# Kernel optimization log

Hardware: AMD Instinct MI355X
Metric: run time of the kernel (lower is better)

The kernel has to match this reference:

```python
import jax, jax.numpy as jnp
import numpy as np
import math

D_MODEL = 1024
N_HEADS = 16
FACTOR = 5
B, L, S = 8, 4096, 4096
U = FACTOR * int(math.log(L))  # 40 sampled queries


def setup_inputs() -> dict:
    key = jax.random.key(0)
    ks = jax.random.split(key, 12)
    scale_w = 1.0 / math.sqrt(D_MODEL)
    return {
        "queries": jax.random.normal(ks[0], (B, L, D_MODEL), dtype=jnp.float32),
        "keys": jax.random.normal(ks[1], (B, S, D_MODEL), dtype=jnp.float32),
        "values": jax.random.normal(ks[2], (B, S, D_MODEL), dtype=jnp.float32),
        "Wq": jax.random.normal(ks[3], (D_MODEL, D_MODEL), dtype=jnp.float32) * scale_w,
        "bq": jnp.zeros((D_MODEL,), dtype=jnp.float32),
        "Wk": jax.random.normal(ks[4], (D_MODEL, D_MODEL), dtype=jnp.float32) * scale_w,
        "bk": jnp.zeros((D_MODEL,), dtype=jnp.float32),
        "Wv": jax.random.normal(ks[5], (D_MODEL, D_MODEL), dtype=jnp.float32) * scale_w,
        "bv": jnp.zeros((D_MODEL,), dtype=jnp.float32),
        "Wo": jax.random.normal(ks[6], (D_MODEL, D_MODEL), dtype=jnp.float32) * scale_w,
        "bo": jnp.zeros((D_MODEL,), dtype=jnp.float32),
        "sample_index": jax.random.randint(ks[7], (U,), 0, L, dtype=jnp.int64 if jax.config.jax_enable_x64 else jnp.int32),
    }


def reference(queries, keys, values, Wq, bq, Wk, bk, Wv, bv, Wo, bo, sample_index):
    H, E = N_HEADS, D_MODEL // N_HEADS
    scale = D_MODEL ** (-0.5)  # module uses d_model**-0.5, not d_head**-0.5

    # Projections (torch Linear: y = x @ W.T + b)
    Q = (jnp.einsum('bld,od->blo', queries, Wq) + bq).reshape(B, L, H, E)
    K = (jnp.einsum('bsd,od->bso', keys, Wk) + bk).reshape(B, S, H, E)
    V = (jnp.einsum('bsd,od->bso', values, Wv) + bv).reshape(B, S, H, E)

    # ProbSparse query sampling: gather U = factor*log(L) queries
    Qs = Q[:, sample_index, :, :]  # [B, U, H, E]

    # SDPA on the reduced query set
    scores = jnp.einsum('buhe,bshe->bhus', Qs, K) * scale  # [B, H, U, S]
    attn = jax.nn.softmax(scores, axis=-1)
    out = jnp.einsum('bhus,bshe->buhe', attn, V).reshape(B, U, D_MODEL)

    out = jnp.einsum('bud,od->buo', out, Wo) + bo  # [B, U, D_MODEL]
    return out, attn
```

## Files before the change

### kernel.cpp

```cpp
#include <hip/hip_runtime.h>
#include <stdint.h>

#define DM  1024
#define NB  8
#define LQ  4096
#define SSQ 4096
#define NH  16
#define HE  64
#define UU  40
#define NS  8
#define SPL (SSQ/NS)

using u16 = unsigned short;
using u32 = unsigned int;

typedef __bf16 bf16x8 __attribute__((ext_vector_type(8)));
typedef float  f32x4  __attribute__((ext_vector_type(4)));

#define AS1 __attribute__((address_space(1)))
#define AS3 __attribute__((address_space(3)))

__device__ __forceinline__ void gld_lds16(const void* g, void* l) {
  __builtin_amdgcn_global_load_lds((const AS1 u32*)g, (AS3 u32*)l, 16, 0, 0);
}

__device__ __forceinline__ u16 f2bf(float x) {
  u32 u = __float_as_uint(x);
  u32 r = (u + 0x7fffu + ((u >> 16) & 1u)) >> 16;
  return (u16)r;
}

__global__ __launch_bounds__(256)
void conv_bf16(const float* __restrict__ src, u16* __restrict__ dst, long n) {
  long i = ((long)blockIdx.x * 256 + threadIdx.x) * 8;
  if (i >= n) return;
  float4 a = *(const float4*)(src + i);
  float4 b = *(const float4*)(src + i + 4);
  union { u16 h[8]; uint4 v; } pk;
  pk.h[0]=f2bf(a.x); pk.h[1]=f2bf(a.y); pk.h[2]=f2bf(a.z); pk.h[3]=f2bf(a.w);
  pk.h[4]=f2bf(b.x); pk.h[5]=f2bf(b.y); pk.h[6]=f2bf(b.z); pk.h[7]=f2bf(b.w);
  *(uint4*)(dst + i) = pk.v;
}

struct WPtrs {
  const float* s0; const float* s1; const float* s2; const float* s3;
  u16* d0; u16* d1; u16* d2; u16* d3;
};
__global__ __launch_bounds__(256)
void conv_w4(WPtrs p) {
  int wsel = blockIdx.y;
  const float* s = wsel==0 ? p.s0 : wsel==1 ? p.s1 : wsel==2 ? p.s2 : p.s3;
  u16*         d = wsel==0 ? p.d0 : wsel==1 ? p.d1 : wsel==2 ? p.d2 : p.d3;
  long i = ((long)blockIdx.x * 256 + threadIdx.x) * 8;
  float4 a = *(const float4*)(s + i);
  float4 b = *(const float4*)(s + i + 4);
  union { u16 h[8]; uint4 v; } pk;
  pk.h[0]=f2bf(a.x); pk.h[1]=f2bf(a.y); pk.h[2]=f2bf(a.z); pk.h[3]=f2bf(a.w);
  pk.h[4]=f2bf(b.x); pk.h[5]=f2bf(b.y); pk.h[6]=f2bf(b.z); pk.h[7]=f2bf(b.w);
  *(uint4*)(d + i) = pk.v;
}

__global__ __launch_bounds__(128)
void gather_q_bf16(const float* __restrict__ q, const int* __restrict__ sidx,
                   u16* __restrict__ dst) {
  int r = blockIdx.x;
  int b = r / UU, u = r - b*UU;
  long srow = ((long)b*LQ + sidx[u]) * DM;
  int c = threadIdx.x * 8;
  float4 a = *(const float4*)(q + srow + c);
  float4 bb = *(const float4*)(q + srow + c + 4);
  union { u16 h[8]; uint4 v; } pk;
  pk.h[0]=f2bf(a.x); pk.h[1]=f2bf(a.y); pk.h[2]=f2bf(a.z); pk.h[3]=f2bf(a.w);
  pk.h[4]=f2bf(bb.x); pk.h[5]=f2bf(bb.y); pk.h[6]=f2bf(bb.z); pk.h[7]=f2bf(bb.w);
  *(uint4*)(dst + (long)r*DM + c) = pk.v;
}

template<bool BIAS_ROW, bool MINOR_N>
__global__ __launch_bounds__(512, 2)
void gemm256(const u16* __restrict__ Ab, const u16* __restrict__ Bb,
             const float* __restrict__ bias, u16* __restrict__ Cb,
             int mTiles, int nTiles, long ldo)
{
  __shared__ u16 lds[2][2][256*64];
  const int t = threadIdx.x;
  const int l = t & 63;
  const int w = t >> 6;
  const int wr = w >> 2, wc = w & 3;

  const int nwg = mTiles * nTiles;
  const int bid = blockIdx.x;
  const int wg = (bid & 7) * (nwg >> 3) + (bid >> 3);
  int xm, yn;
  if (MINOR_N) { xm = wg / nTiles; yn = wg - xm*nTiles; }
  else         { yn = wg / mTiles; xm = wg - yn*mTiles; }
  const int r0 = xm * 256, o0 = yn * 256;

  const int srow = t >> 3, sslot = t & 7;
  const int scol = (sslot ^ (srow & 7)) * 8;
  const long aoff = (long)(r0 + srow) * DM + scol;
  const long boff = (long)(o0 + srow) * DM + scol;

  f32x4 acc[8][4];
  const f32x4 z4 = {0.f,0.f,0.f,0.f};
#pragma unroll
  for (int m = 0; m < 8; m++)
#pragma unroll
    for (int n = 0; n < 4; n++) acc[m][n] = z4;

  const int swz   = (l & 7) << 4;
  const int klane = (l >> 4) << 4;
  const int arow0 = wr*128 + (l & 15);
  const int brow0 = wc*64  + (l & 15);

  auto stage = [&](int tile, int buf) {
#pragma unroll
    for (int j = 0; j < 4; j++)
      gld_lds16(Ab + aoff + (long)j*(64*DM) + tile*64,
                (char*)&lds[buf][0][0] + (512*j + 64*w)*16);
#pragma unroll
    for (int j = 0; j < 4; j++)
      gld_lds16(Bb + boff + (long)j*(64*DM) + tile*64,
                (char*)&lds[buf][1][0] + (512*j + 64*w)*16);
  };

  stage(0, 0);
  __syncthreads();

  for (int tt = 0; tt < 16; tt++) {
    const int cur = tt & 1;
    if (tt < 15) stage(tt+1, cur^1);
    const char* Abase = (const char*)&lds[cur][0][0];
    const char* Bbase = (const char*)&lds[cur][1][0];
#pragma unroll
    for (int kk = 0; kk < 2; kk++) {
      const int cb = (kk*64 + klane) ^ swz;
      bf16x8 af[8], bf[4];
#pragma unroll
      for (int m = 0; m < 8; m++)
        af[m] = *(const bf16x8*)(Abase + (arow0 + m*16)*128 + cb);
#pragma unroll
      for (int n = 0; n < 4; n++)
        bf[n] = *(const bf16x8*)(Bbase + (brow0 + n*16)*128 + cb);
      __builtin_amdgcn_s_setprio(1);
#pragma unroll
      for (int m = 0; m < 8; m++)
#pragma unroll
        for (int n = 0; n < 4; n++)
          acc[m][n] = __builtin_amdgcn_mfma_f32_16x16x32_bf16(af[m], bf[n], acc[m][n], 0, 0, 0);
      __builtin_amdgcn_s_setprio(0);
    }
    __syncthreads();
  }

  float* eps = (float*)((char*)&lds[0][0][0] + w*8704);
  const int colg = o0 + wc*64 + (l & 7)*8;
  float bc[8];
  if (!BIAS_ROW) {
    float4 b0 = *(const float4*)&bias[colg];
    float4 b1 = *(const float4*)&bias[colg + 4];
    bc[0]=b0.x; bc[1]=b0.y; bc[2]=b0.z; bc[3]=b0.w;
    bc[4]=b1.x; bc[5]=b1.y; bc[6]=b1.z; bc[7]=b1.w;
  }
  const int fq = l >> 4;
  const int fr16 = l & 15;
#pragma unroll
  for (int mc = 0; mc < 4; mc++) {
#pragma unroll
    for (int mm = 0; mm < 2; mm++) {
      int m = mc*2 + mm;
#pragma unroll
      for (int n = 0; n < 4; n++)
#pragma unroll
        for (int i2 = 0; i2 < 4; i2++)
          eps[(mm*16 + fq*4 + i2)*68 + n*16 + fr16] = acc[m][n][i2];
    }
#pragma unroll
    for (int p = 0; p < 4; p++) {
      int lr = p*8 + (l >> 3);
      int rg = r0 + wr*128 + mc*32 + lr;
      const float* sp = &eps[lr*68 + (l & 7)*8];
      float4 v0 = *(const float4*)sp;
      float4 v1 = *(const float4*)(sp + 4);
      float br = BIAS_ROW ? bias[rg] : 0.f;
      float vv[8] = {v0.x,v0.y,v0.z,v0.w,v1.x,v1.y,v1.z,v1.w};
      union { u16 h[8]; uint4 u; } pk;
#pragma unroll
      for (int q2 = 0; q2 < 8; q2++)
        pk.h[q2] = f2bf(vv[q2] + (BIAS_ROW ? br : bc[q2]));
      *(uint4*)&Cb[(long)rg*ldo + colg] = pk.u;
    }
  }
}

template<bool OUT_BF16, bool BIAS_ROW>
__global__ __launch_bounds__(256)
void gemm_mfma(const u16* __restrict__ Xb, const u16* __restrict__ Wb,
               const float* __restrict__ bias, void* __restrict__ outp,
               int R, long ldo)
{
  __shared__ u16 As[128*40];
  __shared__ u16 Bs[128*40];
  const int t = threadIdx.x;
  const int l = t & 63;
  const int w = t >> 6;
  const int r0 = blockIdx.x * 128;
  const int o0 = blockIdx.y * 128;

  const u16* gsrc[5];
  char* ldst[5];
#pragma unroll
  for (int i = 0; i < 5; i++) {
    int c  = i*256 + t;
    int cb = i*256 + w*64;
    bool a = (cb < 640);
    int cc2 = a ? c : (c - 640);
    int row = cc2 / 5, col = cc2 % 5; if (col > 3) col = 0;
    if (a) {
      int rr = r0 + row; if (rr > R-1) rr = R-1;
      gsrc[i] = Xb + (long)rr * DM + col*8;
      ldst[i] = (char*)As + cb*16;
    } else {
      gsrc[i] = Wb + (long)(o0 + row) * DM + col*8;
      ldst[i] = (char*)Bs + (cb - 640)*16;
    }
  }

  f32x4 acc[4][4];
  const f32x4 z4 = {0.f, 0.f, 0.f, 0.f};
#pragma unroll
  for (int mt = 0; mt < 4; mt++)
#pragma unroll
    for (int nt = 0; nt < 4; nt++) acc[mt][nt] = z4;

  const int rw = (w >> 1) * 64;
  const int cw = (w & 1) * 64;
  const int fr = l & 15;
  const int fk = (l >> 4) * 8;

  for (int k0 = 0; k0 < DM; k0 += 32) {
    __syncthreads();
#pragma unroll
    for (int i = 0; i < 5; i++)
      gld_lds16(gsrc[i] + k0, ldst[i]);
    __syncthreads();

    bf16x8 af[4], bf[4];
#pragma unroll
    for (int mt = 0; mt < 4; mt++)
      af[mt] = *(const bf16x8*)&As[(rw + mt*16 + fr)*40 + fk];
#pragma unroll
    for (int nt = 0; nt < 4; nt++)
      bf[nt] = *(const bf16x8*)&Bs[(cw + nt*16 + fr)*40 + fk];
#pragma unroll
    for (int mt = 0; mt < 4; mt++)
#pragma unroll
      for (int nt = 0; nt < 4; nt++)
        acc[mt][nt] = __builtin_amdgcn_mfma_f32_16x16x32_bf16(af[mt], bf[nt], acc[mt][nt], 0, 0, 0);
  }

  const int colBase = o0 + cw + (l & 15);
  const int rowBase = r0 + rw + ((l >> 4) << 2);
#pragma unroll
  for (int nt = 0; nt < 4; nt++) {
    float bvc = BIAS_ROW ? 0.f : bias[colBase + nt*16];
#pragma unroll
    for (int mt = 0; mt < 4; mt++) {
#pragma unroll
      for (int i2 = 0; i2 < 4; i2++) {
        int r = rowBase + mt*16 + i2;
        if (r < R) {
          float v = acc[mt][nt][i2] + (BIAS_ROW ? bias[r] : bvc);
          long o = (long)r*ldo + colBase + nt*16;
          if (OUT_BF16) ((u16*)outp)[o] = f2bf(v);
          else          ((float*)outp)[o] = v;
        }
      }
    }
  }
}

__global__ __launch_bounds__(256)
void attn_stats(const u16* __restrict__ Qs16, const u16* __restrict__ Kb,
                float* __restrict__ STp)
{
  const int h = blockIdx.x, b = blockIdx.y, z = blockIdx.z;
  const int t = threadIdx.x, l = t & 63, w = t >> 6;
  __shared__ float sm4[4][48], sl4[4][48];

  bf16x8 qf[3][2];
#pragma unroll
  for (int mt = 0; mt < 3; mt++) {
    int u = mt*16 + (l & 15); if (u >= UU) u = UU-1;
    const u16* qrow = Qs16 + ((long)b*UU + u)*DM + h*HE + ((l>>4)*8);
    qf[mt][0] = *(const bf16x8*)qrow;
    qf[mt][1] = *(const bf16x8*)(qrow + 32);
  }
  float m_[12], l_[12];
#pragma unroll
  for (int i = 0; i < 12; i++) { m_[i] = -1e30f; l_[i] = 0.f; }

  const f32x4 z4 = {0.f,0.f,0.f,0.f};
  const int sbase = z*SPL + w*128;
  for (int tt = 0; tt < 8; tt++) {
    const int s0 = sbase + tt*16;
    const u16* krow = Kb + ((long)(b*SSQ + s0 + (l & 15)))*DM + h*HE + ((l>>4)*8);
    bf16x8 kf0 = *(const bf16x8*)krow;
    bf16x8 kf1 = *(const bf16x8*)(krow + 32);
    f32x4 as[3];
#pragma unroll
    for (int mt = 0; mt < 3; mt++) {
      as[mt] = __builtin_amdgcn_mfma_f32_16x16x32_bf16(qf[mt][0], kf0, z4, 0, 0, 0);
      as[mt] = __builtin_amdgcn_mfma_f32_16x16x32_bf16(qf[mt][1], kf1, as[mt], 0, 0, 0);
    }
#pragma unroll
    for (int mt = 0; mt < 3; mt++)
#pragma unroll
      for (int i2 = 0; i2 < 4; i2++) {
        int idx = mt*4 + i2;
        float x = as[mt][i2] * 0.03125f;
        float mn = fmaxf(m_[idx], x);
        l_[idx] = l_[idx]*__expf(m_[idx]-mn) + __expf(x-mn);
        m_[idx] = mn;
      }
  }
#pragma unroll
  for (int off = 1; off < 16; off <<= 1)
#pragma unroll
    for (int idx = 0; idx < 12; idx++) {
      float m2 = __shfl_xor(m_[idx], off, 64);
      float l2 = __shfl_xor(l_[idx], off, 64);
      float mn = fmaxf(m_[idx], m2);
      l_[idx] = l_[idx]*__expf(m_[idx]-mn) + l2*__expf(m2-mn);
      m_[idx] = mn;
    }
  if ((l & 15) == 0) {
#pragma unroll
    for (int idx = 0; idx < 12; idx++) {
      int u = (idx>>2)*16 + ((l>>4)<<2) + (idx&3);
      sm4[w][u] = m_[idx]; sl4[w][u] = l_[idx];
    }
  }
  __syncthreads();
  if (t < UU) {
    float M = -1e30f, L = 0.f;
#pragma unroll
    for (int wv = 0; wv < 4; wv++) {
      float m2 = sm4[wv][t], l2 = sl4[wv][t];
      float mn = fmaxf(M, m2);
      L = L*__expf(M-mn) + l2*__expf(m2-mn);
      M = mn;
    }
    long p = (((long)(b*NH + h)*UU + t)*NS + z)*2;
    STp[p] = M; STp[p+1] = L;
  }
}

__global__ __launch_bounds__(256)
void merge_stats(const float* __restrict__ STp, float* __restrict__ ST) {
  int idx = blockIdx.x*256 + threadIdx.x;
  if (idx >= NB*NH*UU) return;
  float M = -1e30f;
#pragma unroll
  for (int z = 0; z < NS; z++) M = fmaxf(M, STp[((long)idx*NS+z)*2]);
  float L = 0.f;
#pragma unroll
  for (int z = 0; z < NS; z++)
    L += STp[((long)idx*NS+z)*2+1] * __expf(STp[((long)idx*NS+z)*2] - M);
  ST[idx*2] = M; ST[idx*2+1] = L;
}

__global__ __launch_bounds__(256, 2)
void attn_pv(const u16* __restrict__ Qs16, const u16* __restrict__ Kb,
             const u16* __restrict__ VTb, const float* __restrict__ ST,
             float* __restrict__ attn, float* __restrict__ ohp)
{
  const int h = blockIdx.x, b = blockIdx.y, z = blockIdx.z;
  const int t = threadIdx.x, l = t & 63, w = t >> 6;
  const long LVT = (long)NB*SSQ;

  __shared__ u16   Plds[4][48*40];
  __shared__ float sM[48], sLi[48];
  __shared__ float red[48][68];

  if (t < 48) {
    if (t < UU) {
      long p = ((long)(b*NH+h)*UU + t)*2;
      sM[t] = ST[p]; sLi[t] = 1.f / ST[p+1];
    } else { sM[t] = 0.f; sLi[t] = 0.f; }
  }
  __syncthreads();

  float Mr[12], Lir[12];
#pragma unroll
  for (int mt = 0; mt < 3; mt++)
#pragma unroll
    for (int i2 = 0; i2 < 4; i2++) {
      int u = mt*16 + ((l>>4)<<2) + i2;
      Mr[mt*4+i2] = sM[u]; Lir[mt*4+i2] = sLi[u];
    }

  bf16x8 qf[3][2];
#pragma unroll
  for (int mt = 0; mt < 3; mt++) {
    int u = mt*16 + (l & 15); if (u >= UU) u = UU-1;
    const u16* qrow = Qs16 + ((long)b*UU + u)*DM + h*HE + ((l>>4)*8);
    qf[mt][0] = *(const bf16x8*)qrow;
    qf[mt][1] = *(const bf16x8*)(qrow + 32);
  }

  f32x4 acc_pv[4][3];
  const f32x4 z4 = {0.f,0.f,0.f,0.f};
#pragma unroll
  for (int et = 0; et < 4; et++)
#pragma unroll
    for (int nt = 0; nt < 3; nt++) acc_pv[et][nt] = z4;

  const int sbase = z*SPL + w*128;
  for (int tt = 0; tt < 4; tt++) {
    const int s0 = sbase + tt*32;
    bf16x8 vf[4];
#pragma unroll
    for (int et = 0; et < 4; et++)
      vf[et] = *(const bf16x8*)(VTb + (long)(h*HE + et*16 + (l&15))*LVT
                                    + (long)b*SSQ + s0 + ((l>>4)*8));
    bf16x8 kf[2][2];
#pragma unroll
    for (int st = 0; st < 2; st++) {
      const u16* krow = Kb + ((long)(b*SSQ + s0 + st*16 + (l & 15)))*DM + h*HE + ((l>>4)*8);
      kf[st][0] = *(const bf16x8*)krow;
      kf[st][1] = *(const bf16x8*)(krow + 32);
    }
#pragma unroll
    for (int st = 0; st < 2; st++) {
      f32x4 as[3];
#pragma unroll
      for (int mt = 0; mt < 3; mt++) {
        as[mt] = __builtin_amdgcn_mfma_f32_16x16x32_bf16(qf[mt][0], kf[st][0], z4, 0, 0, 0);
        as[mt] = __builtin_amdgcn_mfma_f32_16x16x32_bf16(qf[mt][1], kf[st][1], as[mt], 0, 0, 0);
      }
#pragma unroll
      for (int mt = 0; mt < 3; mt++)
#pragma unroll
        for (int i2 = 0; i2 < 4; i2++) {
          int idx = mt*4 + i2;
          int u = mt*16 + ((l>>4)<<2) + i2;
          float p = __expf(as[mt][i2]*0.03125f - Mr[idx]) * Lir[idx];
          if (u < UU)
            attn[((long)((b*NH+h)*UU + u))*SSQ + s0 + st*16 + (l & 15)] = p;
          Plds[w][u*40 + st*16 + (l & 15)] = f2bf(p);
        }
    }
#pragma unroll
    for (int nt = 0; nt < 3; nt++) {
      bf16x8 pb = *(const bf16x8*)&Plds[w][(nt*16 + (l & 15))*40 + ((l>>4)*8)];
#pragma unroll
      for (int et = 0; et < 4; et++)
        acc_pv[et][nt] = __builtin_amdgcn_mfma_f32_16x16x32_bf16(vf[et], pb, acc_pv[et][nt], 0, 0, 0);
    }
  }

  __syncthreads();
  for (int wv = 0; wv < 4; wv++) {
    if (w == wv) {
#pragma unroll
      for (int et = 0; et < 4; et++)
#pragma unroll
        for (int nt = 0; nt < 3; nt++)
#pragma unroll
          for (int i2 = 0; i2 < 4; i2++) {
            int u = nt*16 + (l & 15);
            int e = et*16 + ((l>>4)<<2) + i2;
            if (wv == 0) red[u][e]  = acc_pv[et][nt][i2];
            else         red[u][e] += acc_pv[et][nt][i2];
          }
    }
    __syncthreads();
  }
  for (int idx = t; idx < UU*64; idx += 256) {
    int u = idx >> 6, e = idx & 63;
    ohp[(long)z*((long)NB*UU*DM) + ((long)b*UU + u)*DM + h*HE + e] = red[u][e];
  }
}

__global__ __launch_bounds__(256)
void reduce_oh(const float* __restrict__ ohp, u16* __restrict__ ohb) {
  long i = (long)blockIdx.x*256 + threadIdx.x;
  const long n = (long)NB*UU*DM;
  if (i >= n) return;
  float s = 0.f;
#pragma unroll
  for (int z = 0; z < NS; z++) s += ohp[(long)z*n + i];
  ohb[i] = f2bf(s);
}

extern "C" void kernel_launch(void* const* d_in, const int* in_sizes, int n_in,
                              void* d_out, int out_size, void* d_ws, size_t ws_size,
                              hipStream_t stream)
{
  const float* queries = (const float*)d_in[0];
  const float* keys    = (const float*)d_in[1];
  const float* values  = (const float*)d_in[2];
  const float* Wq = (const float*)d_in[3];
  const float* bq = (const float*)d_in[4];
  const float* Wk = (const float*)d_in[5];
  const float* bk = (const float*)d_in[6];
  const float* Wv = (const float*)d_in[7];
  const float* bv = (const float*)d_in[8];
  const float* Wo = (const float*)d_in[9];
  const float* bo = (const float*)d_in[10];
  const int* sidx = (const int*)d_in[11];

  float* out_main = (float*)d_out;
  float* attn     = out_main + (long)NB*UU*DM;

  const long kvE = (long)NB*SSQ*DM;
  const size_t wB = (size_t)DM*DM*2;

  char* ws = (char*)d_ws;
  u16*  Xst = (u16*)ws;                      ws += (size_t)kvE*2;
  u16*  Kbf = (u16*)ws;                      ws += (size_t)kvE*2;
  u16*  VTb = (u16*)ws;                      ws += (size_t)kvE*2;
  u16*  Wkb = (u16*)ws;                      ws += wB;
  u16*  Wvb = (u16*)ws;                      ws += wB;
  u16*  Wqb = (u16*)ws;                      ws += wB;
  u16*  Wob = (u16*)ws;                      ws += wB;
  u16*  Qgb = (u16*)ws;                      ws += (size_t)NB*UU*DM*2;
  u16*  Qs16= (u16*)ws;                      ws += (size_t)NB*UU*DM*2;
  u16*  OHb = (u16*)ws;                      ws += (size_t)NB*UU*DM*2;
  float* ohp = (float*)ws;                   ws += (size_t)NS*NB*UU*DM*4;
  float* STp = (float*)ws;                   ws += (size_t)NB*NH*UU*NS*2*4;
  float* ST  = (float*)ws;

  dim3 blk(256);
  const long wN = (long)DM*DM;
  dim3 gconvX((kvE/8 + 255)/256);
  dim3 gw4(wN/8/256, 4);
  dim3 gq((NB*UU + 127)/128, DM/128);
  dim3 gat(NH, NB, NS);

  WPtrs wp = { Wk, Wv, Wq, Wo, Wkb, Wvb, Wqb, Wob };
  conv_w4<<<gw4, blk, 0, stream>>>(wp);
  gather_q_bf16<<<NB*UU, 128, 0, stream>>>(queries, sidx, Qgb);

  conv_bf16<<<gconvX, blk, 0, stream>>>(keys, Xst, kvE);
  gemm256<false,true><<<dim3(512), dim3(512), 0, stream>>>(Xst, Wkb, bk, Kbf,
                                                           128, 4, (long)DM);
  conv_bf16<<<gconvX, blk, 0, stream>>>(values, Xst, kvE);
  gemm256<true,false><<<dim3(512), dim3(512), 0, stream>>>(Wvb, Xst, bv, VTb,
                                                           4, 128, (long)NB*SSQ);
  gemm_mfma<true,false><<<gq, blk, 0, stream>>>(Qgb, Wqb, bq, Qs16, NB*UU, DM);

  attn_stats<<<gat, blk, 0, stream>>>(Qs16, Kbf, STp);
  merge_stats<<<(NB*NH*UU + 255)/256, blk, 0, stream>>>(STp, ST);
  attn_pv<<<gat, blk, 0, stream>>>(Qs16, Kbf, VTb, ST, attn, ohp);

  reduce_oh<<<((long)NB*UU*DM + 255)/256, blk, 0, stream>>>(ohp, OHb);
  gemm_mfma<false,false><<<gq, blk, 0, stream>>>(OHb, Wob, bo, out_main, NB*UU, DM);
}
```

Baseline: 654.3 us.

## Fuse fp32-to-bf16 conversion into K/V projection GEMMs and split-K small GEMMs

Removes the separate conversion passes over keys and values. The big projection GEMMs now load fp32 tiles straight into registers, convert them to bf16 and write them into LDS after the MFMA work for the current tile, so the load overlaps compute. This drops a full write and re-read of a 64MB bf16 staging buffer per input. The small Q and output projections are split along K into 4 partial GEMMs plus a combine kernel to raise the number of workgroups, at the cost of an extra partial-sum buffer and launch.

```diff
diff --git a/kernel.cpp b/kernel.cpp
--- a/kernel.cpp
+++ b/kernel.cpp
@@ -10,6 +10,7 @@
 #define UU  40
 #define NS  8
 #define SPL (SSQ/NS)
+#define KS  4
 
 using u16 = unsigned short;
 using u32 = unsigned int;
@@ -28,18 +29,6 @@
   u32 u = __float_as_uint(x);
   u32 r = (u + 0x7fffu + ((u >> 16) & 1u)) >> 16;
   return (u16)r;
-}
-
-__global__ __launch_bounds__(256)
-void conv_bf16(const float* __restrict__ src, u16* __restrict__ dst, long n) {
-  long i = ((long)blockIdx.x * 256 + threadIdx.x) * 8;
-  if (i >= n) return;
-  float4 a = *(const float4*)(src + i);
-  float4 b = *(const float4*)(src + i + 4);
-  union { u16 h[8]; uint4 v; } pk;
-  pk.h[0]=f2bf(a.x); pk.h[1]=f2bf(a.y); pk.h[2]=f2bf(a.z); pk.h[3]=f2bf(a.w);
-  pk.h[4]=f2bf(b.x); pk.h[5]=f2bf(b.y); pk.h[6]=f2bf(b.z); pk.h[7]=f2bf(b.w);
-  *(uint4*)(dst + i) = pk.v;
 }
 
 struct WPtrs {
@@ -75,9 +64,9 @@
   *(uint4*)(dst + (long)r*DM + c) = pk.v;
 }
 
-template<bool BIAS_ROW, bool MINOR_N>
+template<bool A32, bool B32, bool BIAS_ROW, bool MINOR_N>
 __global__ __launch_bounds__(512, 2)
-void gemm256(const u16* __restrict__ Ab, const u16* __restrict__ Bb,
+void gemm256(const void* __restrict__ Ap, const void* __restrict__ Bp,
              const float* __restrict__ bias, u16* __restrict__ Cb,
              int mTiles, int nTiles, long ldo)
 {
@@ -96,9 +85,41 @@
   const int r0 = xm * 256, o0 = yn * 256;
 
   const int srow = t >> 3, sslot = t & 7;
-  const int scol = (sslot ^ (srow & 7)) * 8;
-  const long aoff = (long)(r0 + srow) * DM + scol;
-  const long boff = (long)(o0 + srow) * DM + scol;
+  const int scol  = (sslot ^ (srow & 7)) * 8;
+  const int dslot = (sslot ^ (srow & 7));
+
+  const u16*   Ab  = (const u16*)Ap   + (long)r0*DM;
+  const u16*   Bb  = (const u16*)Bp   + (long)o0*DM;
+  const float* Af  = (const float*)Ap + (long)r0*DM;
+  const float* Bf  = (const float*)Bp + (long)o0*DM;
+
+  float4 vs[8];
+  auto loadS = [&](const float* S, int tile) {
+#pragma unroll
+    for (int j = 0; j < 4; j++) {
+      const float* p = S + (long)(srow + 64*j)*DM + tile*64 + sslot*8;
+      vs[2*j]   = *(const float4*)p;
+      vs[2*j+1] = *(const float4*)(p + 4);
+    }
+  };
+  auto writeS = [&](int op, int buf) {
+#pragma unroll
+    for (int j = 0; j < 4; j++) {
+      float f[8] = {vs[2*j].x, vs[2*j].y, vs[2*j].z, vs[2*j].w,
+                    vs[2*j+1].x, vs[2*j+1].y, vs[2*j+1].z, vs[2*j+1].w};
+      union { u16 h[8]; uint4 u4; } pk;
+#pragma unroll
+      for (int q = 0; q < 8; q++) pk.h[q] = f2bf(f[q]);
+      *(uint4*)&lds[buf][op][(srow + 64*j)*64 + dslot*8] = pk.u4;
+    }
+  };
+  auto stageGld = [&](const u16* S, int op, int tile, int buf) {
+#pragma unroll
+    for (int j = 0; j < 4; j++)
+      gld_lds16(S + (long)(srow + 64*j)*DM + tile*64 + scol - (long)(t>>3)*DM
+                  + (long)(t>>3)*DM,
+                (char*)&lds[buf][op][0] + (512*j + 64*w)*16);
+  };
 
   f32x4 acc[8][4];
   const f32x4 z4 = {0.f,0.f,0.f,0.f};
@@ -112,23 +133,22 @@
   const int arow0 = wr*128 + (l & 15);
   const int brow0 = wc*64  + (l & 15);
 
-  auto stage = [&](int tile, int buf) {
-#pragma unroll
-    for (int j = 0; j < 4; j++)
-      gld_lds16(Ab + aoff + (long)j*(64*DM) + tile*64,
-                (char*)&lds[buf][0][0] + (512*j + 64*w)*16);
-#pragma unroll
-    for (int j = 0; j < 4; j++)
-      gld_lds16(Bb + boff + (long)j*(64*DM) + tile*64,
-                (char*)&lds[buf][1][0] + (512*j + 64*w)*16);
-  };
-
-  stage(0, 0);
+  if (A32) loadS(Af, 0);
+  if (B32) loadS(Bf, 0);
+  if (!A32) stageGld(Ab, 0, 0, 0);
+  if (!B32) stageGld(Bb, 1, 0, 0);
+  if (A32) writeS(0, 0);
+  if (B32) writeS(1, 0);
   __syncthreads();
 
   for (int tt = 0; tt < 16; tt++) {
     const int cur = tt & 1;
-    if (tt < 15) stage(tt+1, cur^1);
+    if (tt < 15) {
+      if (A32) loadS(Af, tt+1);
+      if (B32) loadS(Bf, tt+1);
+      if (!A32) stageGld(Ab, 0, tt+1, cur^1);
+      if (!B32) stageGld(Bb, 1, tt+1, cur^1);
+    }
     const char* Abase = (const char*)&lds[cur][0][0];
     const char* Bbase = (const char*)&lds[cur][1][0];
 #pragma unroll
@@ -148,6 +168,10 @@
         for (int n = 0; n < 4; n++)
           acc[m][n] = __builtin_amdgcn_mfma_f32_16x16x32_bf16(af[m], bf[n], acc[m][n], 0, 0, 0);
       __builtin_amdgcn_s_setprio(0);
+    }
+    if (tt < 15) {
+      if (A32) writeS(0, cur^1);
+      if (B32) writeS(1, cur^1);
     }
     __syncthreads();
   }
@@ -183,20 +207,18 @@
       float4 v1 = *(const float4*)(sp + 4);
       float br = BIAS_ROW ? bias[rg] : 0.f;
       float vv[8] = {v0.x,v0.y,v0.z,v0.w,v1.x,v1.y,v1.z,v1.w};
-      union { u16 h[8]; uint4 u; } pk;
+      union { u16 h[8]; uint4 u4; } pk;
 #pragma unroll
       for (int q2 = 0; q2 < 8; q2++)
         pk.h[q2] = f2bf(vv[q2] + (BIAS_ROW ? br : bc[q2]));
-      *(uint4*)&Cb[(long)rg*ldo + colg] = pk.u;
-    }
-  }
-}
-
-template<bool OUT_BF16, bool BIAS_ROW>
+      *(uint4*)&Cb[(long)rg*ldo + colg] = pk.u4;
+    }
+  }
+}
+
 __global__ __launch_bounds__(256)
-void gemm_mfma(const u16* __restrict__ Xb, const u16* __restrict__ Wb,
-               const float* __restrict__ bias, void* __restrict__ outp,
-               int R, long ldo)
+void gemm_small_sk(const u16* __restrict__ Xb, const u16* __restrict__ Wb,
+                   float* __restrict__ pout, int R)
 {
   __shared__ u16 As[128*40];
   __shared__ u16 Bs[128*40];
@@ -205,6 +227,7 @@
   const int w = t >> 6;
   const int r0 = blockIdx.x * 128;
   const int o0 = blockIdx.y * 128;
+  const int kz = blockIdx.z;
 
   const u16* gsrc[5];
   char* ldst[5];
@@ -237,7 +260,7 @@
   const int fr = l & 15;
   const int fk = (l >> 4) * 8;
 
-  for (int k0 = 0; k0 < DM; k0 += 32) {
+  for (int k0 = kz*(DM/KS); k0 < (kz+1)*(DM/KS); k0 += 32) {
     __syncthreads();
 #pragma unroll
     for (int i = 0; i < 5; i++)
@@ -260,23 +283,31 @@
 
   const int colBase = o0 + cw + (l & 15);
   const int rowBase = r0 + rw + ((l >> 4) << 2);
-#pragma unroll
-  for (int nt = 0; nt < 4; nt++) {
-    float bvc = BIAS_ROW ? 0.f : bias[colBase + nt*16];
-#pragma unroll
-    for (int mt = 0; mt < 4; mt++) {
+  float* pz = pout + (long)kz*R*DM;
+#pragma unroll
+  for (int nt = 0; nt < 4; nt++)
+#pragma unroll
+    for (int mt = 0; mt < 4; mt++)
 #pragma unroll
       for (int i2 = 0; i2 < 4; i2++) {
         int r = rowBase + mt*16 + i2;
-        if (r < R) {
-          float v = acc[mt][nt][i2] + (BIAS_ROW ? bias[r] : bvc);
-          long o = (long)r*ldo + colBase + nt*16;
-          if (OUT_BF16) ((u16*)outp)[o] = f2bf(v);
-          else          ((float*)outp)[o] = v;
-        }
+        if (r < R) pz[(long)r*DM + colBase + nt*16] = acc[mt][nt][i2];
       }
-    }
-  }
+}
+
+template<bool OUT_BF16>
+__global__ __launch_bounds__(256)
+void combine_sk(const float* __restrict__ p, const float* __restrict__ bias,
+                void* __restrict__ out, int R)
+{
+  long n = (long)R*DM;
+  long i = (long)blockIdx.x*256 + threadIdx.x;
+  if (i >= n) return;
+  float s = bias[i & (DM-1)];
+#pragma unroll
+  for (int z = 0; z < KS; z++) s += p[(long)z*n + i];
+  if (OUT_BF16) ((u16*)out)[i] = f2bf(s);
+  else          ((float*)out)[i] = s;
 }
 
 __global__ __launch_bounds__(256)
@@ -515,45 +546,48 @@
 
   const long kvE = (long)NB*SSQ*DM;
   const size_t wB = (size_t)DM*DM*2;
+  const int  RQ = NB*UU;
 
   char* ws = (char*)d_ws;
-  u16*  Xst = (u16*)ws;                      ws += (size_t)kvE*2;
   u16*  Kbf = (u16*)ws;                      ws += (size_t)kvE*2;
   u16*  VTb = (u16*)ws;                      ws += (size_t)kvE*2;
   u16*  Wkb = (u16*)ws;                      ws += wB;
   u16*  Wvb = (u16*)ws;                      ws += wB;
   u16*  Wqb = (u16*)ws;                      ws += wB;
   u16*  Wob = (u16*)ws;                      ws += wB;
-  u16*  Qgb = (u16*)ws;                      ws += (size_t)NB*UU*DM*2;
-  u16*  Qs16= (u16*)ws;                      ws += (size_t)NB*UU*DM*2;
-  u16*  OHb = (u16*)ws;                      ws += (size_t)NB*UU*DM*2;
+  u16*  Qgb = (u16*)ws;                      ws += (size_t)RQ*DM*2;
+  u16*  Qs16= (u16*)ws;                      ws += (size_t)RQ*DM*2;
+  u16*  OHb = (u16*)ws;                      ws += (size_t)RQ*DM*2;
+  float* pbuf= (float*)ws;                   ws += (size_t)KS*RQ*DM*4;
   float* ohp = (float*)ws;                   ws += (size_t)NS*NB*UU*DM*4;
   float* STp = (float*)ws;                   ws += (size_t)NB*NH*UU*NS*2*4;
   float* ST  = (float*)ws;
 
   dim3 blk(256);
   const long wN = (long)DM*DM;
-  dim3 gconvX((kvE/8 + 255)/256);
   dim3 gw4(wN/8/256, 4);
-  dim3 gq((NB*UU + 127)/128, DM/128);
+  dim3 gsk((RQ + 127)/128, DM/128, KS);
+  dim3 gcmb(((long)RQ*DM + 255)/256);
   dim3 gat(NH, NB, NS);
 
   WPtrs wp = { Wk, Wv, Wq, Wo, Wkb, Wvb, Wqb, Wob };
   conv_w4<<<gw4, blk, 0, stream>>>(wp);
-  gather_q_bf16<<<NB*UU, 128, 0, stream>>>(queries, sidx, Qgb);
-
-  conv_bf16<<<gconvX, blk, 0, stream>>>(keys, Xst, kvE);
-  gemm256<false,true><<<dim3(512), dim3(512), 0, stream>>>(Xst, Wkb, bk, Kbf,
-                                                           128, 4, (long)DM);
-  conv_bf16<<<gconvX, blk, 0, stream>>>(values, Xst, kvE);
-  gemm256<true,false><<<dim3(512), dim3(512), 0, stream>>>(Wvb, Xst, bv, VTb,
-                                                           4, 128, (long)NB*SSQ);
-  gemm_mfma<true,false><<<gq, blk, 0, stream>>>(Qgb, Wqb, bq, Qs16, NB*UU, DM);
+  gather_q_bf16<<<RQ, 128, 0, stream>>>(queries, sidx, Qgb);
+
+  gemm256<true,false,false,true><<<dim3(512), dim3(512), 0, stream>>>(
+      keys, Wkb, bk, Kbf, 128, 4, (long)DM);
+  gemm256<false,true,true,false><<<dim3(512), dim3(512), 0, stream>>>(
+      Wvb, values, bv, VTb, 4, 128, (long)NB*SSQ);
+
+  gemm_small_sk<<<gsk, blk, 0, stream>>>(Qgb, Wqb, pbuf, RQ);
+  combine_sk<true><<<gcmb, blk, 0, stream>>>(pbuf, bq, Qs16, RQ);
 
   attn_stats<<<gat, blk, 0, stream>>>(Qs16, Kbf, STp);
   merge_stats<<<(NB*NH*UU + 255)/256, blk, 0, stream>>>(STp, ST);
   attn_pv<<<gat, blk, 0, stream>>>(Qs16, Kbf, VTb, ST, attn, ohp);
 
   reduce_oh<<<((long)NB*UU*DM + 255)/256, blk, 0, stream>>>(ohp, OHb);
-  gemm_mfma<false,false><<<gq, blk, 0, stream>>>(OHb, Wob, bo, out_main, NB*UU, DM);
-}
+
+  gemm_small_sk<<<gsk, blk, 0, stream>>>(OHb, Wob, pbuf, RQ);
+  combine_sk<false><<<gcmb, blk, 0, stream>>>(pbuf, bo, out_main, RQ);
+}
```

Measured after the change: 624.1 us. 4.6% less time.
